# Kernel tuning notes

Measured on AMD Instinct MI355X. Metric: run time of the kernel, lower is better.

Reference implementation:

```python
import jax, jax.numpy as jnp
import numpy as np
import math

N = 50000        # nodes
DEG = 16         # regular out-degree -> E = N*DEG edges, grouped by source node
B = 64           # graphs in batch
F = 128          # num_node_features
H = 128          # nhid == enhid
RATIO = 0.5      # edge_ratio
NUM_CONVS = 3
E = N * DEG


def setup_inputs() -> dict:
    key = jax.random.key(0)
    ks = jax.random.split(key, 18)
    s = 0.05
    x = jax.random.normal(ks[0], (N, F), jnp.float32)
    edge_src = jnp.repeat(jnp.arange(N, dtype=jnp.int32), DEG)          # sorted by src
    edge_dst = jax.random.randint(ks[1], (E,), 0, N, jnp.int32)
    batch = ((jnp.arange(N) * B) // N).astype(jnp.int32)                 # sorted graph ids
    edge_attr = jnp.ones((E, 1), jnp.float32)                            # edge_attr=None branch
    inp = {"x": x, "edge_attr": edge_attr, "edge_src": edge_src,
           "edge_dst": edge_dst, "batch": batch}
    # GCNConv weights: [F->H, H->H, H->H]
    inp["W_gcn0"] = jax.random.normal(ks[2], (F, H), jnp.float32) * s
    inp["b_gcn0"] = jnp.zeros((H,), jnp.float32)
    inp["W_gcn1"] = jax.random.normal(ks[3], (H, H), jnp.float32) * s
    inp["b_gcn1"] = jnp.zeros((H,), jnp.float32)
    inp["W_gcn2"] = jax.random.normal(ks[4], (H, H), jnp.float32) * s
    inp["b_gcn2"] = jnp.zeros((H,), jnp.float32)
    # EGNN edge convs: [1->H, H->H]
    inp["W_eg0"] = jax.random.normal(ks[5], (1, H), jnp.float32) * s
    inp["b_eg0"] = jnp.zeros((H,), jnp.float32)
    inp["W_eg1"] = jax.random.normal(ks[6], (H, H), jnp.float32) * s
    inp["b_eg1"] = jnp.zeros((H,), jnp.float32)
    # score convs: [H->1, H->1]
    inp["W_sc0"] = jax.random.normal(ks[7], (H, 1), jnp.float32) * s
    inp["b_sc0"] = jnp.zeros((1,), jnp.float32)
    inp["W_sc1"] = jax.random.normal(ks[8], (H, 1), jnp.float32) * s
    inp["b_sc1"] = jnp.zeros((1,), jnp.float32)
    return inp


def _gcn(x, src, dst, ew, W, b):
    # PyG GCNConv: add self-loops (weight 1), symmetric deg normalization, aggregate at dst.
    n = x.shape[0]
    loop = jnp.arange(n, dtype=src.dtype)
    src2 = jnp.concatenate([src, loop])
    dst2 = jnp.concatenate([dst, loop])
    ew2 = jnp.concatenate([ew, jnp.ones((n,), ew.dtype)])
    deg = jax.ops.segment_sum(ew2, dst2, n)
    dinv = jnp.where(deg > 0, jax.lax.rsqrt(jnp.maximum(deg, 1e-12)), 0.0)
    norm = dinv[src2] * dinv[dst2] * ew2                                  # [E+n]
    msg = (x @ W)[src2] * norm[:, None]                                    # gather + scale
    return jax.ops.segment_sum(msg, dst2, n) + b                           # scatter-add


def _egnn(e, src, W, b):
    # Edge conv: scatter edge features to their source node, gather back, linear map.
    agg = jax.ops.segment_sum(e, src, N)
    return agg[src] @ W + b


def _pool(h, batch):
    gmax = jax.ops.segment_max(h, batch, B)
    gsum = jax.ops.segment_sum(h, batch, B)
    cnt = jax.ops.segment_sum(jnp.ones((h.shape[0],), h.dtype), batch, B)
    gmean = gsum / cnt[:, None]
    return jnp.concatenate([gmax, gmean, gsum], axis=1)                    # [B, 3H]


def reference(x, edge_attr, edge_src, edge_dst, batch,
              W_gcn0, b_gcn0, W_gcn1, b_gcn1, W_gcn2, b_gcn2,
              W_eg0, b_eg0, W_eg1, b_eg1, W_sc0, b_sc0, W_sc1, b_sc1):
    gW = [W_gcn0, W_gcn1, W_gcn2]
    gb = [b_gcn0, b_gcn1, b_gcn2]
    eW = [W_eg0, W_eg1]
    eb = [b_eg0, b_eg1]
    sW = [W_sc0, W_sc1]
    sb = [b_sc0, b_sc1]
    src, dst = edge_src, edge_dst
    deg = DEG
    ew = jnp.ones((src.shape[0],), jnp.float32)
    h = x
    ea = edge_attr
    xs = jnp.zeros((B, 3 * H), jnp.float32)
    for i in range(NUM_CONVS):
        h = jax.nn.relu(_gcn(h, src, dst, ew, gW[i], gb[i]))
        if i < NUM_CONVS - 1:
            ea = jax.nn.relu(_egnn(ea, src, eW[i], eb[i]))
            score = jnp.tanh(_egnn(ea, src, sW[i], sb[i])[:, 0])           # [E_cur]
            k = math.ceil(RATIO * deg)                                      # per-src-node top-k
            vals, idx = jax.lax.top_k(score.reshape(N, deg), k)             # [N,k]
            dst = jnp.take_along_axis(dst.reshape(N, deg), idx, axis=1).reshape(-1)
            flat = (jnp.arange(N)[:, None] * deg + idx).reshape(-1)
            ea = ea[flat]
            src = jnp.repeat(jnp.arange(N, dtype=src.dtype), k)
            ew = jnp.clip(vals.reshape(-1), 0.0, 1.0)
            deg = k
        xs = xs + _pool(h, batch)
    return xs
```

## Files before the change

### kernel.cpp

```cpp
#include <hip/hip_runtime.h>
#include <math.h>

#define NNODES 50000
#define DEGREE 16
#define NGRAPH 64
#define CAP 64
#define LDA 136
#define NXCD 8
#define XRANGE (NNODES / NXCD)
#define NTILE 782
#define ACHUNK 784
#define BCAP 192

typedef unsigned short u16;
typedef unsigned int u32;
typedef unsigned long long u64;
using short8 = __attribute__((ext_vector_type(8))) short;
using f32x4  = __attribute__((ext_vector_type(4))) float;
using fv4    = __attribute__((ext_vector_type(4))) float;

__device__ __forceinline__ u16 f2bf(float f) {
  union { float f; u32 u; } v; v.f = f;
  u32 u = v.u;
  return (u16)((u + 0x7FFFu + ((u >> 16) & 1u)) >> 16);
}
__device__ __forceinline__ float2 bf2x2(u32 u) {
  union { u32 u; float f; } lo, hi;
  lo.u = (u & 0xFFFFu) << 16; hi.u = u & 0xFFFF0000u;
  return make_float2(lo.f, hi.f);
}
__device__ __forceinline__ u32 pack2(float x, float y) {
  return (u32)f2bf(x) | ((u32)f2bf(y) << 16);
}
__device__ __forceinline__ int lowerb(const int* b, int n, int v) {
  int lo = 0, hi = n;
  while (lo < hi) { int m = (lo + hi) >> 1; if (b[m] < v) lo = m + 1; else hi = m; }
  return lo;
}

__device__ __forceinline__ void cons8(uint4 v, float w, float* acc) {
  float2 p;
  p = bf2x2(v.x); acc[0] = fmaf(w, p.x, acc[0]); acc[1] = fmaf(w, p.y, acc[1]);
  p = bf2x2(v.y); acc[2] = fmaf(w, p.x, acc[2]); acc[3] = fmaf(w, p.y, acc[3]);
  p = bf2x2(v.z); acc[4] = fmaf(w, p.x, acc[4]); acc[5] = fmaf(w, p.y, acc[5]);
  p = bf2x2(v.w); acc[6] = fmaf(w, p.x, acc[6]); acc[7] = fmaf(w, p.y, acc[7]);
}
__device__ __forceinline__ void consP(uint4 v, float* mx, float* sm) {
  float2 p;
  p = bf2x2(v.x);
  mx[0] = fmaxf(mx[0], p.x); sm[0] += p.x; mx[1] = fmaxf(mx[1], p.y); sm[1] += p.y;
  p = bf2x2(v.y);
  mx[2] = fmaxf(mx[2], p.x); sm[2] += p.x; mx[3] = fmaxf(mx[3], p.y); sm[3] += p.y;
  p = bf2x2(v.z);
  mx[4] = fmaxf(mx[4], p.x); sm[4] += p.x; mx[5] = fmaxf(mx[5], p.y); sm[5] += p.y;
  p = bf2x2(v.w);
  mx[6] = fmaxf(mx[6], p.x); sm[6] += p.x; mx[7] = fmaxf(mx[7], p.y); sm[7] += p.y;
}

__global__ __launch_bounds__(256) void k_init(
    const float* __restrict__ eattr,
    const float* __restrict__ weg, const float* __restrict__ beg,
    const float* __restrict__ wsc, const float* __restrict__ bsc,
    const float* __restrict__ W0, const float* __restrict__ W1,
    const float* __restrict__ W2, const float* __restrict__ W3,
    float* __restrict__ ew1, float* __restrict__ agg0, u16* __restrict__ Wt,
    const int* __restrict__ edst, int* __restrict__ cnt,
    int* __restrict__ slots, int2* __restrict__ stag, int* __restrict__ scnt) {
  __shared__ int2 lbuf[NXCD * BCAP];
  __shared__ int lcnt[NXCD];
  int b = blockIdx.x, t = threadIdx.x;
  if (b < 196) {
    int i = b * 256 + t;
    if (i < NNODES) {
      const fv4* p = reinterpret_cast<const fv4*>(eattr + (size_t)i * DEGREE);
      float s = 0.f;
#pragma unroll
      for (int j = 0; j < 4; ++j) {
        fv4 w = __builtin_nontemporal_load(&p[j]);
        s += w.x + w.y + w.z + w.w;
      }
      agg0[i] = s;
      float sc = 0.f;
      for (int k = 0; k < 128; ++k) {
        float e = fmaxf(fmaf(s, weg[k], beg[k]), 0.f);
        sc = fmaf(e, wsc[k], sc);
      }
      float v1 = tanhf(fmaf(16.f, sc, bsc[0]));
      ew1[i] = fminf(fmaxf(v1, 0.f), 1.f);
    }
  } else if (b < 452) {
    int idx = (b - 196) * 256 + t;
    int which = idx >> 14, r = idx & 16383;
    int k = r >> 7, n = r & 127;
    const float* W = which == 0 ? W0 : which == 1 ? W1 : which == 2 ? W2 : W3;
    Wt[which * 16384 + n * 128 + k] = f2bf(W[k * 128 + n]);
  } else {
    int b2 = b - 452;
    if (t < NXCD) lcnt[t] = 0;
    __syncthreads();
    int e0 = b2 * ACHUNK;
    for (int k = 0; k < ACHUNK; k += 256) {
      int idx = k + t;
      int e = e0 + idx;
      if (idx < ACHUNK && e < NNODES * DEGREE) {
        int d = edst[e];
        u32 r = (u32)d / (u32)XRANGE;
        int pos = atomicAdd(&lcnt[r], 1);
        if (pos < BCAP) {
          lbuf[r * BCAP + pos] = make_int2(e, d);
        } else {
          int gp = atomicAdd(&cnt[d], 1);
          if (gp < CAP) slots[(size_t)d * CAP + gp] = e;
        }
      }
    }
    __syncthreads();
    for (int idx = t; idx < NXCD * BCAP; idx += 256) {
      int r = idx / BCAP, i = idx - r * BCAP;
      if (i < min(lcnt[r], BCAP))
        stag[((size_t)r * 1024 + b2) * BCAP + i] = lbuf[idx];
    }
    if (t < NXCD) scnt[t * 1024 + b2] = min(lcnt[t], BCAP);
  }
}

__global__ __launch_bounds__(256) void k_gemmF(
    int nFill, const int2* __restrict__ stag, const int* __restrict__ scnt,
    int* __restrict__ cnt, int* __restrict__ slots,
    int nGemm, const u16* __restrict__ A, const float* __restrict__ Af32,
    const u16* __restrict__ WtA, u16* __restrict__ outA,
    int nEg, const float* __restrict__ agg0, const float* __restrict__ weg,
    const float* __restrict__ beg, const u16* __restrict__ WtE,
    const float* __restrict__ beE, const float* __restrict__ wsc1,
    const float* __restrict__ bs1, float* __restrict__ ewOut) {
  __shared__ u16 Bs[128 * LDA];
  int b = blockIdx.x, t = threadIdx.x;
  int nWork = nGemm + nEg;
  if (b >= nWork) {
    int f = b - nWork;
    int r = f & (NXCD - 1), sub = f >> 3;
    for (int q = 0; q < 8; ++q) {
      int sb = sub * 8 + q;
      int c = scnt[r * 1024 + sb];
      const int2* src = &stag[((size_t)r * 1024 + sb) * BCAP];
      for (int i = t; i < c; i += 256) {
        int2 v = src[i];
        int pos = atomicAdd(&cnt[v.y], 1);
        if (pos < CAP) slots[(size_t)v.y * CAP + pos] = v.x;
      }
    }
    return;
  }
  int eg = (b >= nGemm);
  const u16* Wsrc = eg ? WtE : WtA;
  for (int i = t; i < 2048; i += 256) {
    int r = i >> 4, c = (i & 15) << 3;
    *reinterpret_cast<uint4*>(&Bs[r * LDA + c]) =
        *reinterpret_cast<const uint4*>(&Wsrc[r * 128 + c]);
  }
  int m0 = (eg ? (b - nGemm) : b) * 64;
  int wave = t >> 6, lane = t & 63;
  int lm = lane & 15, quad = lane >> 4;
  int row = m0 + wave * 16 + lm;
  short8 af[4];
  if (eg) {
    float a = (row < NNODES) ? agg0[row] : 0.f;
#pragma unroll
    for (int kc = 0; kc < 4; ++kc) {
      int k0 = kc * 32 + quad * 8;
      float v[8];
#pragma unroll
      for (int j = 0; j < 8; ++j)
        v[j] = 8.f * fmaxf(fmaf(a, weg[k0 + j], beg[k0 + j]), 0.f);
      uint4 o;
      o.x = pack2(v[0], v[1]); o.y = pack2(v[2], v[3]);
      o.z = pack2(v[4], v[5]); o.w = pack2(v[6], v[7]);
      af[kc] = *reinterpret_cast<short8*>(&o);
    }
  } else if (Af32) {
    if (row < NNODES) {
      const fv4* px = reinterpret_cast<const fv4*>(Af32 + (size_t)row * 128);
#pragma unroll
      for (int kc = 0; kc < 4; ++kc) {
        int k0 = (kc * 32 + quad * 8) >> 2;
        fv4 v0 = __builtin_nontemporal_load(&px[k0]);
        fv4 v1 = __builtin_nontemporal_load(&px[k0 + 1]);
        uint4 o;
        o.x = pack2(v0.x, v0.y); o.y = pack2(v0.z, v0.w);
        o.z = pack2(v1.x, v1.y); o.w = pack2(v1.z, v1.w);
        af[kc] = *reinterpret_cast<short8*>(&o);
      }
    } else {
      uint4 o = make_uint4(0u, 0u, 0u, 0u);
#pragma unroll
      for (int kc = 0; kc < 4; ++kc) af[kc] = *reinterpret_cast<short8*>(&o);
    }
  } else {
    if (row < NNODES) {
#pragma unroll
      for (int kc = 0; kc < 4; ++kc)
        af[kc] = *reinterpret_cast<const short8*>(
            &A[(size_t)row * 128 + kc * 32 + quad * 8]);
    } else {
      uint4 o = make_uint4(0u, 0u, 0u, 0u);
#pragma unroll
      for (int kc = 0; kc < 4; ++kc) af[kc] = *reinterpret_cast<short8*>(&o);
    }
  }
  __syncthreads();
  f32x4 z = {0.f, 0.f, 0.f, 0.f};
  f32x4 acc[8];
#pragma unroll
  for (int n = 0; n < 8; ++n) acc[n] = z;
#pragma unroll
  for (int kc = 0; kc < 4; ++kc) {
#pragma unroll
    for (int n = 0; n < 8; ++n) {
      short8 bf = *reinterpret_cast<const short8*>(
          &Bs[(n * 16 + lm) * LDA + kc * 32 + quad * 8]);
      acc[n] = __builtin_amdgcn_mfma_f32_16x16x32_bf16(af[kc], bf, acc[n], 0, 0, 0);
    }
  }
  if (!eg) {
#pragma unroll
    for (int n = 0; n < 8; ++n) {
      int col = n * 16 + lm;
#pragma unroll
      for (int r = 0; r < 4; ++r) {
        int orow = m0 + wave * 16 + quad * 4 + r;
        if (orow < NNODES) outA[(size_t)orow * 128 + col] = f2bf(acc[n][r]);
      }
    }
  } else {
    float s0 = 0.f, s1 = 0.f, s2 = 0.f, s3 = 0.f;
#pragma unroll
    for (int n = 0; n < 8; ++n) {
      int col = n * 16 + lm;
      float bb2 = beE[col], wv = wsc1[col];
      s0 = fmaf(fmaxf(acc[n][0] + bb2, 0.f), wv, s0);
      s1 = fmaf(fmaxf(acc[n][1] + bb2, 0.f), wv, s1);
      s2 = fmaf(fmaxf(acc[n][2] + bb2, 0.f), wv, s2);
      s3 = fmaf(fmaxf(acc[n][3] + bb2, 0.f), wv, s3);
    }
#pragma unroll
    for (int m = 8; m >= 1; m >>= 1) {
      s0 += __shfl_xor(s0, m, 64);
      s1 += __shfl_xor(s1, m, 64);
      s2 += __shfl_xor(s2, m, 64);
      s3 += __shfl_xor(s3, m, 64);
    }
    if (lm == 0) {
      float bsv = bs1[0];
      float sv[4] = {s0, s1, s2, s3};
#pragma unroll
      for (int r = 0; r < 4; ++r) {
        int orow = m0 + wave * 16 + quad * 4 + r;
        if (orow < NNODES) {
          float v = tanhf(fmaf(8.f, sv[r], bsv));
          ewOut[orow] = fminf(fmaxf(v, 0.f), 1.f);
        }
      }
    }
  }
}

template <int MODE>
__global__ __launch_bounds__(256) void k_agg(
    int nAgg, const u16* __restrict__ xwb, const int* __restrict__ cnt,
    const int* __restrict__ slots, const float* __restrict__ wsrc,
    const float* __restrict__ dinv, const float* __restrict__ bias,
    u16* __restrict__ hout,
    const u16* __restrict__ hpool, const int* __restrict__ batch,
    float* __restrict__ out,
    const float* __restrict__ ew1g, float* __restrict__ dv1,
    float* __restrict__ ws1,
    const float* __restrict__ ew2g, float* __restrict__ dv2,
    float* __restrict__ ws2) {
  constexpr int keep = (MODE == 0) ? 16 : (MODE == 1) ? 8 : 4;
  constexpr bool L0 = (MODE == 0);
  constexpr int poolAdd = (MODE >= 2);
  __shared__ float P[1024];
  int b = blockIdx.x, t = threadIdx.x;
  int lane = t & 63;
  int q = lane >> 4, li = lane & 15;
  if (b < nAgg) {
    int n = (b * 256 + t) >> 6;
    if (n >= NNODES) return;
    int c = min(cnt[n], CAP);
    u32 e = 0;
    if (lane < c) e = (u32)slots[(size_t)n * CAP + lane];
    if (L0) {
      u32 j = e & 15u; int srcn = (int)(e >> 4);
      float e1 = 0.f, e2 = 0.f;
      if (lane < c && j < 8u) {
        e1 = ew1g[srcn];
        if (j < 4u) e2 = ew2g[srcn];
      }
#pragma unroll
      for (int m = 32; m >= 1; m >>= 1) {
        e1 += __shfl_xor(e1, m, 64);
        e2 += __shfl_xor(e2, m, 64);
      }
      if (lane == 0) {
        float d1 = rsqrtf(1.0f + e1), d2 = rsqrtf(1.0f + e2);
        dv1[n] = d1; ws1[n] = d1 * ew1g[n];
        dv2[n] = d2; ws2[n] = d2 * ew2g[n];
      }
    }
    int kc; u32 ce;
    if (keep < 16) {
      bool valid = (lane < c) && ((e & 15u) < (u32)keep);
      u64 mask = __ballot(valid);
      kc = (int)__popcll(mask);
      u64 lt = ((u64)1 << lane) - 1;
      int pos = valid ? (int)__popcll(mask & lt) : 63 - (int)__popcll((~mask) & lt);
      ce = (u32)__builtin_amdgcn_ds_permute(pos << 2, (int)e);
    } else { kc = c; ce = e; }
    int sl = 0; float wl = 0.f;
    if (lane < kc) {
      sl = (int)(ce >> 4);
      wl = L0 ? rsqrtf(1.0f + (float)min(cnt[sl], CAP)) : wsrc[sl];
    }
    const uint4* b4 = reinterpret_cast<const uint4*>(xwb);
    uint4 selfv = b4[n * 16 + li];
    float acc[8] = {0.f, 0.f, 0.f, 0.f, 0.f, 0.f, 0.f, 0.f};
    for (int i = 0; i < kc; i += 16) {
      int r0 = i + q, r1 = i + 4 + q, r2 = i + 8 + q, r3 = i + 12 + q;
      int s0 = __shfl(sl, r0, 64); float w0 = __shfl(wl, r0, 64);
      int s1 = __shfl(sl, r1, 64); float w1 = __shfl(wl, r1, 64);
      int s2 = __shfl(sl, r2, 64); float w2 = __shfl(wl, r2, 64);
      int s3 = __shfl(sl, r3, 64); float w3 = __shfl(wl, r3, 64);
      if (r0 >= kc) { s0 = n; w0 = 0.f; }
      if (r1 >= kc) { s1 = n; w1 = 0.f; }
      if (r2 >= kc) { s2 = n; w2 = 0.f; }
      if (r3 >= kc) { s3 = n; w3 = 0.f; }
      uint4 v0 = b4[s0 * 16 + li];
      uint4 v1 = selfv, v2 = selfv, v3 = selfv;
      if (i + 4 < kc)  v1 = b4[s1 * 16 + li];
      if (i + 8 < kc)  v2 = b4[s2 * 16 + li];
      if (i + 12 < kc) v3 = b4[s3 * 16 + li];
      cons8(v0, w0, acc);
      cons8(v1, w1, acc);
      cons8(v2, w2, acc);
      cons8(v3, w3, acc);
    }
#pragma unroll
    for (int k = 0; k < 8; ++k) {
      acc[k] += __shfl_xor(acc[k], 16, 64);
      acc[k] += __shfl_xor(acc[k], 32, 64);
    }
    float di = L0 ? rsqrtf(1.0f + (float)c) : dinv[n];
    float dd = di * di;
    const f32x4* bp = reinterpret_cast<const f32x4*>(bias);
    f32x4 bv0 = bp[li * 2], bv1 = bp[li * 2 + 1];
    float2 p0 = bf2x2(selfv.x), p1 = bf2x2(selfv.y),
           p2 = bf2x2(selfv.z), p3 = bf2x2(selfv.w);
    float r0 = fmaxf(fmaf(di, acc[0], fmaf(dd, p0.x, bv0.x)), 0.f);
    float r1 = fmaxf(fmaf(di, acc[1], fmaf(dd, p0.y, bv0.y)), 0.f);
    float r2 = fmaxf(fmaf(di, acc[2], fmaf(dd, p1.x, bv0.z)), 0.f);
    float r3 = fmaxf(fmaf(di, acc[3], fmaf(dd, p1.y, bv0.w)), 0.f);
    float r4 = fmaxf(fmaf(di, acc[4], fmaf(dd, p2.x, bv1.x)), 0.f);
    float r5 = fmaxf(fmaf(di, acc[5], fmaf(dd, p2.y, bv1.y)), 0.f);
    float r6 = fmaxf(fmaf(di, acc[6], fmaf(dd, p3.x, bv1.z)), 0.f);
    float r7 = fmaxf(fmaf(di, acc[7], fmaf(dd, p3.y, bv1.w)), 0.f);
    if (q == 0) {
      uint4 o;
      o.x = pack2(r0, r1); o.y = pack2(r2, r3);
      o.z = pack2(r4, r5); o.w = pack2(r6, r7);
      reinterpret_cast<uint4*>(hout + (size_t)n * 128)[li] = o;
    }
  } else {
    int g = b - nAgg;
    int wv = t >> 6;
    int lo = lowerb(batch, NNODES, g);
    int hi = lowerb(batch, NNODES, g + 1);
    const uint4* hb4 = reinterpret_cast<const uint4*>(hpool);
    float mx[8] = {0.f, 0.f, 0.f, 0.f, 0.f, 0.f, 0.f, 0.f};
    float sm[8] = {0.f, 0.f, 0.f, 0.f, 0.f, 0.f, 0.f, 0.f};
    int n = lo + wv * 4 + q;
    for (; n + 48 < hi; n += 64) {
      uint4 v0 = hb4[(size_t)n * 16 + li];
      uint4 v1 = hb4[(size_t)(n + 16) * 16 + li];
      uint4 v2 = hb4[(size_t)(n + 32) * 16 + li];
      uint4 v3 = hb4[(size_t)(n + 48) * 16 + li];
      consP(v0, mx, sm); consP(v1, mx, sm);
      consP(v2, mx, sm); consP(v3, mx, sm);
    }
    for (; n < hi; n += 16) {
      uint4 v = hb4[(size_t)n * 16 + li];
      consP(v, mx, sm);
    }
#pragma unroll
    for (int k = 0; k < 8; ++k) {
      mx[k] = fmaxf(mx[k], __shfl_xor(mx[k], 16, 64));
      mx[k] = fmaxf(mx[k], __shfl_xor(mx[k], 32, 64));
      sm[k] += __shfl_xor(sm[k], 16, 64);
      sm[k] += __shfl_xor(sm[k], 32, 64);
    }
    if (q == 0) {
#pragma unroll
      for (int k = 0; k < 8; ++k) {
        P[(wv * 16 + li) * 16 + k] = mx[k];
        P[(wv * 16 + li) * 16 + 8 + k] = sm[k];
      }
    }
    __syncthreads();
    if (t < 128) {
      int li2 = t >> 3, k = t & 7;
      int o0 = li2 * 16 + k, o1 = o0 + 8;
      float m = fmaxf(fmaxf(P[o0], P[256 + o0]),
                      fmaxf(P[512 + o0], P[768 + o0]));
      float s = P[o1] + P[256 + o1] + P[512 + o1] + P[768 + o1];
      float cf = (float)(hi - lo);
      int col = li2 * 8 + k;
      float* og = out + g * 384;
      if (poolAdd) {
        og[col] += m; og[128 + col] += s / cf; og[256 + col] += s;
      } else {
        og[col] = m;  og[128 + col] = s / cf;  og[256 + col] = s;
      }
    }
  }
}

extern "C" void kernel_launch(void* const* d_in, const int* in_sizes, int n_in,
                              void* d_out, int out_size, void* d_ws, size_t ws_size,
                              hipStream_t stream) {
  const float* x     = (const float*)d_in[0];
  const float* eattr = (const float*)d_in[1];
  const int*   edst  = (const int*)d_in[3];
  const int*   batch = (const int*)d_in[4];
  const float* Wg0 = (const float*)d_in[5];  const float* bg0 = (const float*)d_in[6];
  const float* Wg1 = (const float*)d_in[7];  const float* bg1 = (const float*)d_in[8];
  const float* Wg2 = (const float*)d_in[9];  const float* bg2 = (const float*)d_in[10];
  const float* We0 = (const float*)d_in[11]; const float* be0 = (const float*)d_in[12];
  const float* We1 = (const float*)d_in[13]; const float* be1 = (const float*)d_in[14];
  const float* Ws0 = (const float*)d_in[15]; const float* bs0 = (const float*)d_in[16];
  const float* Ws1 = (const float*)d_in[17]; const float* bs1 = (const float*)d_in[18];
  float* out = (float*)d_out;

  char* ws = (char*)d_ws;
  const size_t NBH = (size_t)NNODES * 128 * 2;
  size_t off = 0;
  auto alloc = [&](size_t bytes) { void* p = ws + off; off = (off + bytes + 255) & ~(size_t)255; return p; };
  u16*   XWb   = (u16*)alloc(NBH);
  u16*   Hb0   = (u16*)alloc(NBH);
  u16*   Hb1   = (u16*)alloc(NBH);
  u16*   Hb2   = (u16*)alloc(NBH);
  u16*   Wtb   = (u16*)alloc(4 * 128 * 128 * 2);
  int*   slots = (int*)alloc((size_t)NNODES * CAP * 4);
  int*   cnt   = (int*)alloc((size_t)NNODES * 4);
  int2*  stag  = (int2*)alloc((size_t)NXCD * 1024 * BCAP * 8);
  int*   scnt  = (int*)alloc((size_t)NXCD * 1024 * 4);
  float* agg0  = (float*)alloc((size_t)NNODES * 4);
  float* ew1   = (float*)alloc((size_t)NNODES * 4);
  float* ew2   = (float*)alloc((size_t)NNODES * 4);
  float* dinv1 = (float*)alloc((size_t)NNODES * 4);
  float* wsrc1 = (float*)alloc((size_t)NNODES * 4);
  float* dinv2 = (float*)alloc((size_t)NNODES * 4);
  float* wsrc2 = (float*)alloc((size_t)NNODES * 4);

  hipMemsetAsync(cnt, 0, (size_t)NNODES * 4, stream);
  k_init<<<1476, 256, 0, stream>>>(eattr, We0, be0, Ws0, bs0,
                                   Wg0, Wg1, Wg2, We1, ew1, agg0, Wtb,
                                   edst, cnt, slots, stag, scnt);
  k_gemmF<<<2 * NTILE + 1024, 256, 0, stream>>>(
      1024, stag, scnt, cnt, slots,
      NTILE, nullptr, x, Wtb, XWb,
      NTILE, agg0, We0, be0, Wtb + 3 * 16384, be1, Ws1, bs1, ew2);
  k_agg<0><<<12500, 256, 0, stream>>>(12500, XWb, cnt, slots, nullptr, nullptr,
                                      bg0, Hb0, nullptr, batch, nullptr,
                                      ew1, dinv1, wsrc1, ew2, dinv2, wsrc2);
  k_gemmF<<<NTILE, 256, 0, stream>>>(
      0, nullptr, nullptr, nullptr, nullptr,
      NTILE, Hb0, nullptr, Wtb + 16384, XWb,
      0, nullptr, nullptr, nullptr, nullptr, nullptr, nullptr, nullptr, nullptr);
  k_agg<1><<<12500 + NGRAPH, 256, 0, stream>>>(12500, XWb, cnt, slots, wsrc1,
                                               dinv1, bg1, Hb1, Hb0, batch, out,
                                               nullptr, nullptr, nullptr,
                                               nullptr, nullptr, nullptr);
  k_gemmF<<<NTILE, 256, 0, stream>>>(
      0, nullptr, nullptr, nullptr, nullptr,
      NTILE, Hb1, nullptr, Wtb + 2 * 16384, XWb,
      0, nullptr, nullptr, nullptr, nullptr, nullptr, nullptr, nullptr, nullptr);
  k_agg<2><<<12500 + NGRAPH, 256, 0, stream>>>(12500, XWb, cnt, slots, wsrc2,
                                               dinv2, bg2, Hb2, Hb1, batch, out,
                                               nullptr, nullptr, nullptr,
                                               nullptr, nullptr, nullptr);
  k_agg<3><<<NGRAPH, 256, 0, stream>>>(0, nullptr, cnt, slots, nullptr, nullptr,
                                       nullptr, nullptr, Hb2, batch, out,
                                       nullptr, nullptr, nullptr,
                                       nullptr, nullptr, nullptr);
}
```

Baseline: 303.1 us.

## Store node features in column-chunked layout and split aggregation by chunk

```diff
diff --git a/kernel.cpp b/kernel.cpp
--- a/kernel.cpp
+++ b/kernel.cpp
@@ -11,6 +11,8 @@
 #define NTILE 782
 #define ACHUNK 784
 #define BCAP 192
+#define CH ((size_t)NNODES * 32)
+#define NN4 ((size_t)NNODES * 4)
 
 typedef unsigned short u16;
 typedef unsigned int u32;
@@ -36,14 +38,6 @@
   int lo = 0, hi = n;
   while (lo < hi) { int m = (lo + hi) >> 1; if (b[m] < v) lo = m + 1; else hi = m; }
   return lo;
-}
-
-__device__ __forceinline__ void cons8(uint4 v, float w, float* acc) {
-  float2 p;
-  p = bf2x2(v.x); acc[0] = fmaf(w, p.x, acc[0]); acc[1] = fmaf(w, p.y, acc[1]);
-  p = bf2x2(v.y); acc[2] = fmaf(w, p.x, acc[2]); acc[3] = fmaf(w, p.y, acc[3]);
-  p = bf2x2(v.z); acc[4] = fmaf(w, p.x, acc[4]); acc[5] = fmaf(w, p.y, acc[5]);
-  p = bf2x2(v.w); acc[6] = fmaf(w, p.x, acc[6]); acc[7] = fmaf(w, p.y, acc[7]);
 }
 __device__ __forceinline__ void consP(uint4 v, float* mx, float* sm) {
   float2 p;
@@ -62,7 +56,7 @@
     const float* __restrict__ weg, const float* __restrict__ beg,
     const float* __restrict__ wsc, const float* __restrict__ bsc,
     const float* __restrict__ W0, const float* __restrict__ W1,
-    const float* __restrict__ W2, const float* __restrict__ W3,
+    const float* __restrict__ W2,
     float* __restrict__ ew1, float* __restrict__ agg0, u16* __restrict__ Wt,
     const int* __restrict__ edst, int* __restrict__ cnt,
     int* __restrict__ slots, int2* __restrict__ stag, int* __restrict__ scnt) {
@@ -88,14 +82,14 @@
       float v1 = tanhf(fmaf(16.f, sc, bsc[0]));
       ew1[i] = fminf(fmaxf(v1, 0.f), 1.f);
     }
-  } else if (b < 452) {
+  } else if (b < 388) {
     int idx = (b - 196) * 256 + t;
     int which = idx >> 14, r = idx & 16383;
     int k = r >> 7, n = r & 127;
-    const float* W = which == 0 ? W0 : which == 1 ? W1 : which == 2 ? W2 : W3;
+    const float* W = which == 0 ? W0 : which == 1 ? W1 : W2;
     Wt[which * 16384 + n * 128 + k] = f2bf(W[k * 128 + n]);
   } else {
-    int b2 = b - 452;
+    int b2 = b - 388;
     if (t < NXCD) lcnt[t] = 0;
     __syncthreads();
     int e0 = b2 * ACHUNK;
@@ -125,19 +119,42 @@
 }
 
 __global__ __launch_bounds__(256) void k_gemmF(
-    int nFill, const int2* __restrict__ stag, const int* __restrict__ scnt,
-    int* __restrict__ cnt, int* __restrict__ slots,
+    int nEw, const float* __restrict__ agg0, const float* __restrict__ weg,
+    const float* __restrict__ beg, const float* __restrict__ We1f,
+    const float* __restrict__ be1, const float* __restrict__ wsc1,
+    const float* __restrict__ bs1, float* __restrict__ ewOut,
     int nGemm, const u16* __restrict__ A, const float* __restrict__ Af32,
     const u16* __restrict__ WtA, u16* __restrict__ outA,
-    int nEg, const float* __restrict__ agg0, const float* __restrict__ weg,
-    const float* __restrict__ beg, const u16* __restrict__ WtE,
-    const float* __restrict__ beE, const float* __restrict__ wsc1,
-    const float* __restrict__ bs1, float* __restrict__ ewOut) {
+    int nFill, const int2* __restrict__ stag, const int* __restrict__ scnt,
+    int* __restrict__ cnt, int* __restrict__ slots) {
   __shared__ u16 Bs[128 * LDA];
   int b = blockIdx.x, t = threadIdx.x;
-  int nWork = nGemm + nEg;
-  if (b >= nWork) {
-    int f = b - nWork;
+  if (b < nEw) {
+    int i = b * 256 + t;
+    if (i < NNODES) {
+      float a = agg0[i];
+      float sc1 = 0.f;
+      for (int h = 0; h < 2; ++h) {
+        float tt[64];
+#pragma unroll
+        for (int c0 = 0; c0 < 64; ++c0) tt[c0] = 0.f;
+        for (int k = 0; k < 128; ++k) {
+          float e8 = 8.f * fmaxf(fmaf(a, weg[k], beg[k]), 0.f);
+          const float* wr = We1f + k * 128 + h * 64;
+#pragma unroll
+          for (int c0 = 0; c0 < 64; ++c0) tt[c0] = fmaf(e8, wr[c0], tt[c0]);
+        }
+#pragma unroll
+        for (int c0 = 0; c0 < 64; ++c0)
+          sc1 = fmaf(fmaxf(tt[c0] + be1[h * 64 + c0], 0.f), wsc1[h * 64 + c0], sc1);
+      }
+      float v = tanhf(fmaf(8.f, sc1, bs1[0]));
+      ewOut[i] = fminf(fmaxf(v, 0.f), 1.f);
+    }
+    return;
+  }
+  if (b >= nEw + nGemm) {
+    int f = b - nEw - nGemm;
     int r = f & (NXCD - 1), sub = f >> 3;
     for (int q = 0; q < 8; ++q) {
       int sb = sub * 8 + q;
@@ -151,33 +168,18 @@
     }
     return;
   }
-  int eg = (b >= nGemm);
-  const u16* Wsrc = eg ? WtE : WtA;
+  int bb = b - nEw;
   for (int i = t; i < 2048; i += 256) {
     int r = i >> 4, c = (i & 15) << 3;
     *reinterpret_cast<uint4*>(&Bs[r * LDA + c]) =
-        *reinterpret_cast<const uint4*>(&Wsrc[r * 128 + c]);
-  }
-  int m0 = (eg ? (b - nGemm) : b) * 64;
+        *reinterpret_cast<const uint4*>(&WtA[r * 128 + c]);
+  }
+  int m0 = bb * 64;
   int wave = t >> 6, lane = t & 63;
   int lm = lane & 15, quad = lane >> 4;
   int row = m0 + wave * 16 + lm;
   short8 af[4];
-  if (eg) {
-    float a = (row < NNODES) ? agg0[row] : 0.f;
-#pragma unroll
-    for (int kc = 0; kc < 4; ++kc) {
-      int k0 = kc * 32 + quad * 8;
-      float v[8];
-#pragma unroll
-      for (int j = 0; j < 8; ++j)
-        v[j] = 8.f * fmaxf(fmaf(a, weg[k0 + j], beg[k0 + j]), 0.f);
-      uint4 o;
-      o.x = pack2(v[0], v[1]); o.y = pack2(v[2], v[3]);
-      o.z = pack2(v[4], v[5]); o.w = pack2(v[6], v[7]);
-      af[kc] = *reinterpret_cast<short8*>(&o);
-    }
-  } else if (Af32) {
+  if (Af32) {
     if (row < NNODES) {
       const fv4* px = reinterpret_cast<const fv4*>(Af32 + (size_t)row * 128);
 #pragma unroll
@@ -200,7 +202,7 @@
 #pragma unroll
       for (int kc = 0; kc < 4; ++kc)
         af[kc] = *reinterpret_cast<const short8*>(
-            &A[(size_t)row * 128 + kc * 32 + quad * 8]);
+            &A[kc * CH + (size_t)row * 32 + quad * 8]);
     } else {
       uint4 o = make_uint4(0u, 0u, 0u, 0u);
 #pragma unroll
@@ -221,45 +223,13 @@
       acc[n] = __builtin_amdgcn_mfma_f32_16x16x32_bf16(af[kc], bf, acc[n], 0, 0, 0);
     }
   }
-  if (!eg) {
-#pragma unroll
-    for (int n = 0; n < 8; ++n) {
-      int col = n * 16 + lm;
-#pragma unroll
-      for (int r = 0; r < 4; ++r) {
-        int orow = m0 + wave * 16 + quad * 4 + r;
-        if (orow < NNODES) outA[(size_t)orow * 128 + col] = f2bf(acc[n][r]);
-      }
-    }
-  } else {
-    float s0 = 0.f, s1 = 0.f, s2 = 0.f, s3 = 0.f;
-#pragma unroll
-    for (int n = 0; n < 8; ++n) {
-      int col = n * 16 + lm;
-      float bb2 = beE[col], wv = wsc1[col];
-      s0 = fmaf(fmaxf(acc[n][0] + bb2, 0.f), wv, s0);
-      s1 = fmaf(fmaxf(acc[n][1] + bb2, 0.f), wv, s1);
-      s2 = fmaf(fmaxf(acc[n][2] + bb2, 0.f), wv, s2);
-      s3 = fmaf(fmaxf(acc[n][3] + bb2, 0.f), wv, s3);
-    }
-#pragma unroll
-    for (int m = 8; m >= 1; m >>= 1) {
-      s0 += __shfl_xor(s0, m, 64);
-      s1 += __shfl_xor(s1, m, 64);
-      s2 += __shfl_xor(s2, m, 64);
-      s3 += __shfl_xor(s3, m, 64);
-    }
-    if (lm == 0) {
-      float bsv = bs1[0];
-      float sv[4] = {s0, s1, s2, s3};
-#pragma unroll
-      for (int r = 0; r < 4; ++r) {
-        int orow = m0 + wave * 16 + quad * 4 + r;
-        if (orow < NNODES) {
-          float v = tanhf(fmaf(8.f, sv[r], bsv));
-          ewOut[orow] = fminf(fmaxf(v, 0.f), 1.f);
-        }
-      }
+#pragma unroll
+  for (int n = 0; n < 8; ++n) {
+    size_t cb = (size_t)(n >> 1) * CH + (n & 1) * 16 + lm;
+#pragma unroll
+    for (int r = 0; r < 4; ++r) {
+      int orow = m0 + wave * 16 + quad * 4 + r;
+      if (orow < NNODES) outA[cb + (size_t)orow * 32] = f2bf(acc[n][r]);
     }
   }
 }
@@ -276,118 +246,112 @@
     float* __restrict__ ws1,
     const float* __restrict__ ew2g, float* __restrict__ dv2,
     float* __restrict__ ws2) {
-  constexpr int keep = (MODE == 0) ? 16 : (MODE == 1) ? 8 : 4;
+  constexpr u32 KEEP = (MODE == 0) ? 16u : (MODE == 1) ? 8u : 4u;
   constexpr bool L0 = (MODE == 0);
   constexpr int poolAdd = (MODE >= 2);
   __shared__ float P[1024];
   int b = blockIdx.x, t = threadIdx.x;
   int lane = t & 63;
-  int q = lane >> 4, li = lane & 15;
   if (b < nAgg) {
-    int n = (b * 256 + t) >> 6;
-    if (n >= NNODES) return;
+    int chunk = b & 3, nb = b >> 2;
+    int wave = t >> 6;
+    int n = nb * 4 + wave;
+    int r = lane >> 2;
+    int p = lane & 3;
+    size_t cbase = (size_t)chunk * NN4;
+    const uint4* tb4 = reinterpret_cast<const uint4*>(xwb);
     int c = min(cnt[n], CAP);
-    u32 e = 0;
-    if (lane < c) e = (u32)slots[(size_t)n * CAP + lane];
-    if (L0) {
-      u32 j = e & 15u; int srcn = (int)(e >> 4);
-      float e1 = 0.f, e2 = 0.f;
-      if (lane < c && j < 8u) {
-        e1 = ew1g[srcn];
-        if (j < 4u) e2 = ew2g[srcn];
-      }
-#pragma unroll
-      for (int m = 32; m >= 1; m >>= 1) {
-        e1 += __shfl_xor(e1, m, 64);
-        e2 += __shfl_xor(e2, m, 64);
-      }
-      if (lane == 0) {
-        float d1 = rsqrtf(1.0f + e1), d2 = rsqrtf(1.0f + e2);
-        dv1[n] = d1; ws1[n] = d1 * ew1g[n];
-        dv2[n] = d2; ws2[n] = d2 * ew2g[n];
-      }
-    }
-    int kc; u32 ce;
-    if (keep < 16) {
-      bool valid = (lane < c) && ((e & 15u) < (u32)keep);
-      u64 mask = __ballot(valid);
-      kc = (int)__popcll(mask);
-      u64 lt = ((u64)1 << lane) - 1;
-      int pos = valid ? (int)__popcll(mask & lt) : 63 - (int)__popcll((~mask) & lt);
-      ce = (u32)__builtin_amdgcn_ds_permute(pos << 2, (int)e);
-    } else { kc = c; ce = e; }
-    int sl = 0; float wl = 0.f;
-    if (lane < kc) {
-      sl = (int)(ce >> 4);
-      wl = L0 ? rsqrtf(1.0f + (float)min(cnt[sl], CAP)) : wsrc[sl];
-    }
-    const uint4* b4 = reinterpret_cast<const uint4*>(xwb);
-    uint4 selfv = b4[n * 16 + li];
     float acc[8] = {0.f, 0.f, 0.f, 0.f, 0.f, 0.f, 0.f, 0.f};
-    for (int i = 0; i < kc; i += 16) {
-      int r0 = i + q, r1 = i + 4 + q, r2 = i + 8 + q, r3 = i + 12 + q;
-      int s0 = __shfl(sl, r0, 64); float w0 = __shfl(wl, r0, 64);
-      int s1 = __shfl(sl, r1, 64); float w1 = __shfl(wl, r1, 64);
-      int s2 = __shfl(sl, r2, 64); float w2 = __shfl(wl, r2, 64);
-      int s3 = __shfl(sl, r3, 64); float w3 = __shfl(wl, r3, 64);
-      if (r0 >= kc) { s0 = n; w0 = 0.f; }
-      if (r1 >= kc) { s1 = n; w1 = 0.f; }
-      if (r2 >= kc) { s2 = n; w2 = 0.f; }
-      if (r3 >= kc) { s3 = n; w3 = 0.f; }
-      uint4 v0 = b4[s0 * 16 + li];
-      uint4 v1 = selfv, v2 = selfv, v3 = selfv;
-      if (i + 4 < kc)  v1 = b4[s1 * 16 + li];
-      if (i + 8 < kc)  v2 = b4[s2 * 16 + li];
-      if (i + 12 < kc) v3 = b4[s3 * 16 + li];
-      cons8(v0, w0, acc);
-      cons8(v1, w1, acc);
-      cons8(v2, w2, acc);
-      cons8(v3, w3, acc);
-    }
-#pragma unroll
-    for (int k = 0; k < 8; ++k) {
-      acc[k] += __shfl_xor(acc[k], 16, 64);
-      acc[k] += __shfl_xor(acc[k], 32, 64);
-    }
-    float di = L0 ? rsqrtf(1.0f + (float)c) : dinv[n];
+    float e1 = 0.f, e2 = 0.f;
+    for (int i = 0; i < c; i += 16) {
+      int ri = i + r;
+      u32 ent = (u32)slots[(size_t)n * CAP + ri];
+      bool rowv = (ri < c);
+      u32 j = ent & 15u;
+      bool valid = rowv && (j < KEEP);
+      int sv = valid ? (int)(ent >> 4) : n;
+      float wl;
+      if constexpr (L0) {
+        wl = valid ? rsqrtf(1.0f + (float)min(cnt[sv], CAP)) : 0.f;
+        if (chunk == 0 && p == 0 && rowv && j < 8u) {
+          int s2 = (int)(ent >> 4);
+          e1 += ew1g[s2];
+          if (j < 4u) e2 += ew2g[s2];
+        }
+      } else {
+        wl = valid ? wsrc[sv] : 0.f;
+      }
+      uint4 v = tb4[cbase + (size_t)sv * 4 + p];
+      float2 q0 = bf2x2(v.x), q1 = bf2x2(v.y),
+             q2 = bf2x2(v.z), q3 = bf2x2(v.w);
+      acc[0] = fmaf(wl, q0.x, acc[0]); acc[1] = fmaf(wl, q0.y, acc[1]);
+      acc[2] = fmaf(wl, q1.x, acc[2]); acc[3] = fmaf(wl, q1.y, acc[3]);
+      acc[4] = fmaf(wl, q2.x, acc[4]); acc[5] = fmaf(wl, q2.y, acc[5]);
+      acc[6] = fmaf(wl, q3.x, acc[6]); acc[7] = fmaf(wl, q3.y, acc[7]);
+    }
+#pragma unroll
+    for (int m = 4; m <= 32; m <<= 1) {
+#pragma unroll
+      for (int k = 0; k < 8; ++k) acc[k] += __shfl_xor(acc[k], m, 64);
+    }
+    if constexpr (L0) {
+      if (chunk == 0) {
+#pragma unroll
+        for (int m = 4; m <= 32; m <<= 1) {
+          e1 += __shfl_xor(e1, m, 64);
+          e2 += __shfl_xor(e2, m, 64);
+        }
+        if (lane == 0) {
+          float d1 = rsqrtf(1.0f + e1), d2 = rsqrtf(1.0f + e2);
+          dv1[n] = d1; ws1[n] = d1 * ew1g[n];
+          dv2[n] = d2; ws2[n] = d2 * ew2g[n];
+        }
+      }
+    }
+    float di;
+    if constexpr (L0) di = rsqrtf(1.0f + (float)c);
+    else di = dinv[n];
     float dd = di * di;
-    const f32x4* bp = reinterpret_cast<const f32x4*>(bias);
-    f32x4 bv0 = bp[li * 2], bv1 = bp[li * 2 + 1];
-    float2 p0 = bf2x2(selfv.x), p1 = bf2x2(selfv.y),
-           p2 = bf2x2(selfv.z), p3 = bf2x2(selfv.w);
-    float r0 = fmaxf(fmaf(di, acc[0], fmaf(dd, p0.x, bv0.x)), 0.f);
-    float r1 = fmaxf(fmaf(di, acc[1], fmaf(dd, p0.y, bv0.y)), 0.f);
-    float r2 = fmaxf(fmaf(di, acc[2], fmaf(dd, p1.x, bv0.z)), 0.f);
-    float r3 = fmaxf(fmaf(di, acc[3], fmaf(dd, p1.y, bv0.w)), 0.f);
-    float r4 = fmaxf(fmaf(di, acc[4], fmaf(dd, p2.x, bv1.x)), 0.f);
-    float r5 = fmaxf(fmaf(di, acc[5], fmaf(dd, p2.y, bv1.y)), 0.f);
-    float r6 = fmaxf(fmaf(di, acc[6], fmaf(dd, p3.x, bv1.z)), 0.f);
-    float r7 = fmaxf(fmaf(di, acc[7], fmaf(dd, p3.y, bv1.w)), 0.f);
-    if (q == 0) {
+    uint4 sf = tb4[cbase + (size_t)n * 4 + p];
+    const float* bp2 = bias + chunk * 32 + p * 8;
+    fv4 bv0 = *reinterpret_cast<const fv4*>(bp2);
+    fv4 bv1 = *reinterpret_cast<const fv4*>(bp2 + 4);
+    float2 s0 = bf2x2(sf.x), s1 = bf2x2(sf.y), s2 = bf2x2(sf.z), s3 = bf2x2(sf.w);
+    float r0 = fmaxf(fmaf(di, acc[0], fmaf(dd, s0.x, bv0.x)), 0.f);
+    float r1 = fmaxf(fmaf(di, acc[1], fmaf(dd, s0.y, bv0.y)), 0.f);
+    float r2 = fmaxf(fmaf(di, acc[2], fmaf(dd, s1.x, bv0.z)), 0.f);
+    float r3 = fmaxf(fmaf(di, acc[3], fmaf(dd, s1.y, bv0.w)), 0.f);
+    float r4 = fmaxf(fmaf(di, acc[4], fmaf(dd, s2.x, bv1.x)), 0.f);
+    float r5 = fmaxf(fmaf(di, acc[5], fmaf(dd, s2.y, bv1.y)), 0.f);
+    float r6 = fmaxf(fmaf(di, acc[6], fmaf(dd, s3.x, bv1.z)), 0.f);
+    float r7 = fmaxf(fmaf(di, acc[7], fmaf(dd, s3.y, bv1.w)), 0.f);
+    if (r == 0) {
       uint4 o;
       o.x = pack2(r0, r1); o.y = pack2(r2, r3);
       o.z = pack2(r4, r5); o.w = pack2(r6, r7);
-      reinterpret_cast<uint4*>(hout + (size_t)n * 128)[li] = o;
+      reinterpret_cast<uint4*>(hout)[cbase + (size_t)n * 4 + p] = o;
     }
   } else {
     int g = b - nAgg;
     int wv = t >> 6;
+    int q = lane >> 4, li = lane & 15;
     int lo = lowerb(batch, NNODES, g);
     int hi = lowerb(batch, NNODES, g + 1);
     const uint4* hb4 = reinterpret_cast<const uint4*>(hpool);
+    size_t cb = (size_t)(li >> 2) * NN4 + (li & 3);
     float mx[8] = {0.f, 0.f, 0.f, 0.f, 0.f, 0.f, 0.f, 0.f};
     float sm[8] = {0.f, 0.f, 0.f, 0.f, 0.f, 0.f, 0.f, 0.f};
     int n = lo + wv * 4 + q;
     for (; n + 48 < hi; n += 64) {
-      uint4 v0 = hb4[(size_t)n * 16 + li];
-      uint4 v1 = hb4[(size_t)(n + 16) * 16 + li];
-      uint4 v2 = hb4[(size_t)(n + 32) * 16 + li];
-      uint4 v3 = hb4[(size_t)(n + 48) * 16 + li];
+      uint4 v0 = hb4[cb + (size_t)n * 4];
+      uint4 v1 = hb4[cb + (size_t)(n + 16) * 4];
+      uint4 v2 = hb4[cb + (size_t)(n + 32) * 4];
+      uint4 v3 = hb4[cb + (size_t)(n + 48) * 4];
       consP(v0, mx, sm); consP(v1, mx, sm);
       consP(v2, mx, sm); consP(v3, mx, sm);
     }
     for (; n < hi; n += 16) {
-      uint4 v = hb4[(size_t)n * 16 + li];
+      uint4 v = hb4[cb + (size_t)n * 4];
       consP(v, mx, sm);
     }
 #pragma unroll
@@ -412,7 +376,7 @@
                       fmaxf(P[512 + o0], P[768 + o0]));
       float s = P[o1] + P[256 + o1] + P[512 + o1] + P[768 + o1];
       float cf = (float)(hi - lo);
-      int col = li2 * 8 + k;
+      int col = (li2 >> 2) * 32 + (li2 & 3) * 8 + k;
       float* og = out + g * 384;
       if (poolAdd) {
         og[col] += m; og[128 + col] += s / cf; og[256 + col] += s;
@@ -461,29 +425,29 @@
   float* wsrc2 = (float*)alloc((size_t)NNODES * 4);
 
   hipMemsetAsync(cnt, 0, (size_t)NNODES * 4, stream);
-  k_init<<<1476, 256, 0, stream>>>(eattr, We0, be0, Ws0, bs0,
-                                   Wg0, Wg1, Wg2, We1, ew1, agg0, Wtb,
+  k_init<<<1412, 256, 0, stream>>>(eattr, We0, be0, Ws0, bs0,
+                                   Wg0, Wg1, Wg2, ew1, agg0, Wtb,
                                    edst, cnt, slots, stag, scnt);
-  k_gemmF<<<2 * NTILE + 1024, 256, 0, stream>>>(
-      1024, stag, scnt, cnt, slots,
+  k_gemmF<<<196 + NTILE + 1024, 256, 0, stream>>>(
+      196, agg0, We0, be0, We1, be1, Ws1, bs1, ew2,
       NTILE, nullptr, x, Wtb, XWb,
-      NTILE, agg0, We0, be0, Wtb + 3 * 16384, be1, Ws1, bs1, ew2);
-  k_agg<0><<<12500, 256, 0, stream>>>(12500, XWb, cnt, slots, nullptr, nullptr,
+      1024, stag, scnt, cnt, slots);
+  k_agg<0><<<50000, 256, 0, stream>>>(50000, XWb, cnt, slots, nullptr, nullptr,
                                       bg0, Hb0, nullptr, batch, nullptr,
                                       ew1, dinv1, wsrc1, ew2, dinv2, wsrc2);
   k_gemmF<<<NTILE, 256, 0, stream>>>(
-      0, nullptr, nullptr, nullptr, nullptr,
+      0, nullptr, nullptr, nullptr, nullptr, nullptr, nullptr, nullptr, nullptr,
       NTILE, Hb0, nullptr, Wtb + 16384, XWb,
-      0, nullptr, nullptr, nullptr, nullptr, nullptr, nullptr, nullptr, nullptr);
-  k_agg<1><<<12500 + NGRAPH, 256, 0, stream>>>(12500, XWb, cnt, slots, wsrc1,
+      0, nullptr, nullptr, nullptr, nullptr);
+  k_agg<1><<<50000 + NGRAPH, 256, 0, stream>>>(50000, XWb, cnt, slots, wsrc1,
                                                dinv1, bg1, Hb1, Hb0, batch, out,
                                                nullptr, nullptr, nullptr,
                                                nullptr, nullptr, nullptr);
   k_gemmF<<<NTILE, 256, 0, stream>>>(
-      0, nullptr, nullptr, nullptr, nullptr,
+      0, nullptr, nullptr, nullptr, nullptr, nullptr, nullptr, nullptr, nullptr,
       NTILE, Hb1, nullptr, Wtb + 2 * 16384, XWb,
-      0, nullptr, nullptr, nullptr, nullptr, nullptr, nullptr, nullptr, nullptr);
-  k_agg<2><<<12500 + NGRAPH, 256, 0, stream>>>(12500, XWb, cnt, slots, wsrc2,
+      0, nullptr, nullptr, nullptr, nullptr);
+  k_agg<2><<<50000 + NGRAPH, 256, 0, stream>>>(50000, XWb, cnt, slots, wsrc2,
                                                dinv2, bg2, Hb2, Hb1, batch, out,
                                                nullptr, nullptr, nullptr,
                                                nullptr, nullptr, nullptr);
```

Measured after the change: 517.0 us. +70.6%, slower.
